# Kernel tuning notes

Hardware: AMD Instinct MI355X
Metric: run time of the kernel (lower is better)

## Reference

```python
import jax, jax.numpy as jnp
import numpy as np

ALPHA = 0.2   # leaky_relu slope inside GAT/GCN
SLOPE = 0.01  # default F.leaky_relu slope in decoder MLPs


def _leaky(x, s):
    return jnp.where(x > 0, x, s * x)


def _gat(x, mask, W, a, b):
    # AttentionLayer.forward (eval mode: attention dropout off)
    h = x @ W                                   # [N, d]
    d = W.shape[1]
    e = _leaky(h @ a[:d] + (h @ a[d:]).T, ALPHA)  # dense [N, N] scores
    att = jax.nn.softmax(jnp.where(mask > 0, e, -9e15), axis=1)
    out = _leaky(att @ h, ALPHA)
    out = out / jnp.maximum(jnp.linalg.norm(out, axis=1, keepdims=True), 1e-12)  # F.normalize p=2 dim=1
    return out + b


def reference(x, adj, gcn_W, gcn_b, hgat_W, hgat_a, hgat_b, eta,
              l1_W, l1_a, l1_b, l2_W, l2_a, l2_b, l2_rW, l2_rb,
              tf1_W, tf1_b, tf2_W, tf2_b, tg1_W, tg1_b, tg2_W, tg2_b,
              mlp_W, mlp_b, train_sample):
    N = x.shape[0]
    # normalize_adj 'sym' via row/col scaling (avoids diag matmuls)
    rowsum = adj.sum(1)
    dis = rowsum ** -0.5
    dis = jnp.where(jnp.isinf(dis), 0.0, dis)
    gcn_adj = adj * dis[:, None] * dis[None, :]
    # normalize_adj(adj,'rw') is a no-op in the source -> gat_adj = adj + I
    gat_adj = adj + jnp.eye(N, dtype=adj.dtype)

    # HybridLayer (called with gcn_adj for both branches)
    gcn_out = _leaky(gcn_adj @ (x @ gcn_W + gcn_b), 0.2)
    gat_out = _gat(x, gcn_adj, hgat_W, hgat_a, hgat_b)
    h = eta * gcn_out + (1.0 - eta) * gat_out
    h = 0.7 * h + 0.3 * jax.lax.stop_gradient(h)  # x*0.7 + x.detach()*0.3
    h = jax.nn.selu(h)

    # ConvLayer1: ResAttention heads (in==out -> identity residual), mean reduce
    h1 = jnp.mean(jnp.stack([_gat(h, gat_adj, l1_W[i], l1_a[i], l1_b[i]) + h
                             for i in range(l1_W.shape[0])]), axis=0)
    h1 = jax.nn.selu(h1)

    # ConvLayer2: ResAttention heads with linear residual projection, mean reduce
    embed = jnp.mean(jnp.stack([_gat(h1, gat_adj, l2_W[i], l2_a[i], l2_b[i])
                                + (h1 @ l2_rW[i] + l2_rb[i])
                                for i in range(l2_W.shape[0])]), axis=0)

    # decoder MLPs (eval: p=0.01 dropout omitted for determinism)
    tf = _leaky(_leaky(embed @ tf1_W + tf1_b, SLOPE) @ tf2_W + tf2_b, SLOPE)
    tg = _leaky(_leaky(embed @ tg1_W + tg1_b, SLOPE) @ tg2_W + tg2_b, SLOPE)

    pair = jnp.concatenate([tf[train_sample[:, 0]], tg[train_sample[:, 1]]], axis=1)
    return pair @ mlp_W + mlp_b  # type='MLP' decode -> [B, 2]


def setup_inputs() -> dict:
    key = jax.random.key(0)
    ks = jax.random.split(key, 32)
    N, Din, H1, H2, H3, Dout, B, NH = 6144, 512, 256, 128, 64, 32, 4096, 2
    s = 0.05
    r = lambda k, sh: (jax.random.normal(k, sh, jnp.float32) * s)
    adj = (jax.random.uniform(ks[1], (N, N)) < 0.01).astype(jnp.float32)
    return {
        'x': jax.random.normal(ks[0], (N, Din), jnp.float32),
        'adj': adj,
        'gcn_W': r(ks[2], (Din, H1)), 'gcn_b': jnp.zeros((H1,), jnp.float32),
        'hgat_W': r(ks[3], (Din, H1)), 'hgat_a': r(ks[4], (2 * H1, 1)),
        'hgat_b': jnp.zeros((H1,), jnp.float32),
        'eta': jnp.array([0.5], jnp.float32),
        'l1_W': r(ks[5], (NH, H1, H1)), 'l1_a': r(ks[6], (NH, 2 * H1, 1)),
        'l1_b': jnp.zeros((NH, H1), jnp.float32),
        'l2_W': r(ks[7], (NH, H1, H2)), 'l2_a': r(ks[8], (NH, 2 * H2, 1)),
        'l2_b': jnp.zeros((NH, H2), jnp.float32),
        'l2_rW': r(ks[9], (NH, H1, H2)), 'l2_rb': jnp.zeros((NH, H2), jnp.float32),
        'tf1_W': r(ks[10], (H2, H3)), 'tf1_b': jnp.zeros((H3,), jnp.float32),
        'tf2_W': r(ks[11], (H3, Dout)), 'tf2_b': jnp.zeros((Dout,), jnp.float32),
        'tg1_W': r(ks[12], (H2, H3)), 'tg1_b': jnp.zeros((H3,), jnp.float32),
        'tg2_W': r(ks[13], (H3, Dout)), 'tg2_b': jnp.zeros((Dout,), jnp.float32),
        'mlp_W': r(ks[14], (2 * Dout, 2)), 'mlp_b': jnp.zeros((2,), jnp.float32),
        'train_sample': jax.random.randint(ks[15], (B, 2), 0, N, jnp.int32),
    }
```

## Files before the change

kernel.cpp:

```cpp
#include <hip/hip_runtime.h>
#include <math.h>


#define NN 6144
#define CAP 256

typedef __attribute__((ext_vector_type(8))) short bf16x8;
typedef __attribute__((ext_vector_type(4))) float f32x4;

__device__ __forceinline__ unsigned short f2bf(float v) {
  unsigned u = __float_as_uint(v);
  unsigned r = u + 0x7fffu + ((u >> 16) & 1u);
  return (unsigned short)(r >> 16);
}
__device__ __forceinline__ float bf2f(unsigned short h) {
  return __uint_as_float(((unsigned)h) << 16);
}
__device__ __forceinline__ float wave_max(float v) {
#pragma unroll
  for (int off = 32; off > 0; off >>= 1) v = fmaxf(v, __shfl_xor(v, off));
  return v;
}
__device__ __forceinline__ float wave_sum(float v) {
#pragma unroll
  for (int off = 32; off > 0; off >>= 1) v += __shfl_xor(v, off);
  return v;
}
__device__ __forceinline__ float selu_f(float x) {
  const float sc = 1.0507009873554805f, al = 1.6732632423543772f;
  return x > 0.0f ? sc * x : sc * al * (__expf(x) - 1.0f);
}
__device__ __forceinline__ void write_apack4(unsigned short* __restrict__ Ah,
    unsigned short* __restrict__ Al, int KC, int m, int k0,
    float v0, float v1, float v2, float v3) {
  int mt = m >> 4, c = k0 >> 5;
  int lane = ((k0 >> 3) & 3) * 16 + (m & 15);
  int j = k0 & 7;
  size_t base = ((size_t)(mt * KC + c) * 64 + lane) * 8 + j;
  ushort4 hi, lo;
  hi.x = f2bf(v0); lo.x = f2bf(v0 - bf2f(hi.x));
  hi.y = f2bf(v1); lo.y = f2bf(v1 - bf2f(hi.y));
  hi.z = f2bf(v2); lo.z = f2bf(v2 - bf2f(hi.z));
  hi.w = f2bf(v3); lo.w = f2bf(v3 - bf2f(hi.w));
  *(ushort4*)(Ah + base) = hi;
  *(ushort4*)(Al + base) = lo;
}

__global__ __launch_bounds__(256) void build_ell(const float* __restrict__ adj,
    unsigned short* __restrict__ nbr, int* __restrict__ deg,
    int* __restrict__ selfflag, float* __restrict__ dis)
{
  __shared__ unsigned long long mS[4][6][4];
  __shared__ int cntS[4];
  __shared__ int selfS;
  int i = blockIdx.x;
  int t = threadIdx.x, lane = t & 63, w = t >> 6;
  if (t == 0) selfS = 0;
  const float* row = adj + (size_t)i * NN + w * 1536;
  int cnt = 0;
  int hasself = 0;
#pragma unroll
  for (int it = 0; it < 6; ++it) {
    float4 v = *(const float4*)(row + it * 256 + lane * 4);
    unsigned long long m0 = __ballot(v.x != 0.0f);
    unsigned long long m1 = __ballot(v.y != 0.0f);
    unsigned long long m2 = __ballot(v.z != 0.0f);
    unsigned long long m3 = __ballot(v.w != 0.0f);
    if (lane == 0) {
      mS[w][it][0] = m0; mS[w][it][1] = m1; mS[w][it][2] = m2; mS[w][it][3] = m3;
    }
    cnt += __popcll(m0) + __popcll(m1) + __popcll(m2) + __popcll(m3);
  }
  if (lane == 0) cntS[w] = cnt;
  __syncthreads();
  int base = 0;
  for (int ww = 0; ww < w; ++ww) base += cntS[ww];
  unsigned long long below = (1ull << lane) - 1ull;
#pragma unroll
  for (int it = 0; it < 6; ++it) {
    unsigned long long m0 = mS[w][it][0], m1 = mS[w][it][1];
    unsigned long long m2 = mS[w][it][2], m3 = mS[w][it][3];
    int pre = __popcll(m0 & below) + __popcll(m1 & below) +
              __popcll(m2 & below) + __popcll(m3 & below);
    int c = w * 1536 + it * 256 + lane * 4;
    int p = base + pre;
    if ((m0 >> lane) & 1) { if (p < CAP) nbr[(size_t)i * CAP + p] = (unsigned short)c;     if (c == i) hasself = 1; p++; }
    if ((m1 >> lane) & 1) { if (p < CAP) nbr[(size_t)i * CAP + p] = (unsigned short)(c+1); if (c+1 == i) hasself = 1; p++; }
    if ((m2 >> lane) & 1) { if (p < CAP) nbr[(size_t)i * CAP + p] = (unsigned short)(c+2); if (c+2 == i) hasself = 1; p++; }
    if ((m3 >> lane) & 1) { if (p < CAP) nbr[(size_t)i * CAP + p] = (unsigned short)(c+3); if (c+3 == i) hasself = 1; }
    base += __popcll(m0) + __popcll(m1) + __popcll(m2) + __popcll(m3);
  }
  if (hasself) selfS = 1;
  __syncthreads();
  if (t == 0) {
    int total = cntS[0] + cntS[1] + cntS[2] + cntS[3];
    deg[i] = total < CAP ? total : CAP;
    selfflag[i] = selfS;
    dis[i] = (total > 0) ? rsqrtf((float)total) : 0.0f;
  }
}

__global__ __launch_bounds__(256) void pack_all_b(const float* __restrict__ gcn_W,
    const float* __restrict__ hgat_W, const float* __restrict__ l1_W,
    const float* __restrict__ l2_W, const float* __restrict__ l2_rW,
    unsigned short* __restrict__ Bh, unsigned short* __restrict__ Bl)
{
  int idx = blockIdx.x * 256 + threadIdx.x;
  if (idx >= 65536) return;
  const float* B; int K, N, rel;
  if (idx < 32768) {
    B = (idx < 16384) ? gcn_W : hgat_W; K = 512; N = 256; rel = idx & 16383;
  } else if (idx < 49152) {
    B = (idx < 40960) ? l1_W : (l1_W + 65536); K = 256; N = 256; rel = (idx - 32768) & 8191;
  } else {
    int s = (idx - 49152) >> 12;
    B = (s == 0) ? l2_W : (s == 1) ? (l2_W + 32768) : (s == 2) ? l2_rW : (l2_rW + 32768);
    K = 256; N = 128; rel = (idx - 49152) & 4095;
  }
  int l = rel & 63;
  int tc = rel >> 6;
  int KC = K >> 5;
  int c = tc % KC, t = tc / KC;
  int n = t * 16 + (l & 15);
  int kb = c * 32 + (l >> 4) * 8;
  bf16x8 vh, vl;
#pragma unroll
  for (int j = 0; j < 8; ++j) {
    float v = B[(size_t)(kb + j) * N + n];
    unsigned short h = f2bf(v);
    vh[j] = (short)h;
    vl[j] = (short)f2bf(v - bf2f(h));
  }
  *(bf16x8*)(Bh + (size_t)idx * 8) = vh;
  *(bf16x8*)(Bl + (size_t)idx * 8) = vl;
}

__global__ __launch_bounds__(256) void pack_a(const float* __restrict__ A,
    unsigned short* __restrict__ Ah, unsigned short* __restrict__ Al,
    int K, int total)
{
  int idx = blockIdx.x * 256 + threadIdx.x;
  if (idx >= total) return;
  int l = idx & 63;
  int mc = idx >> 6;
  int KC = K >> 5;
  int c = mc % KC, mt = mc / KC;
  int m = mt * 16 + (l & 15);
  int kb = c * 32 + (l >> 4) * 8;
  const float* src = A + (size_t)m * K + kb;
  bf16x8 vh, vl;
#pragma unroll
  for (int j = 0; j < 8; ++j) {
    float v = src[j];
    unsigned short h = f2bf(v);
    vh[j] = (short)h;
    vl[j] = (short)f2bf(v - bf2f(h));
  }
  *(bf16x8*)(Ah + (size_t)idx * 8) = vh;
  *(bf16x8*)(Al + (size_t)idx * 8) = vl;
}

__global__ __launch_bounds__(256) void gemm_mfma(
    const unsigned short* __restrict__ Ah, const unsigned short* __restrict__ Al,
    const unsigned short* __restrict__ Bh, const unsigned short* __restrict__ Bl,
    void* C0, void* C1, void* C2, void* C3,
    const float* b0, const float* b1, const float* b2, const float* b3,
    int KC, int N, long bStride8, int obf16mask)
{
  int z = blockIdx.z;
  void* C = (z == 0) ? C0 : (z == 1) ? C1 : (z == 2) ? C2 : C3;
  const float* bias = (z == 0) ? b0 : (z == 1) ? b1 : (z == 2) ? b2 : b3;
  int obf = (obf16mask >> z) & 1;
  int wave = threadIdx.x >> 6, lane = threadIdx.x & 63;
  int mt = blockIdx.x * 4 + wave;
  int tg0 = blockIdx.y * 2;
  f32x4 acc[2];
  acc[0] = (f32x4){0.f, 0.f, 0.f, 0.f};
  acc[1] = (f32x4){0.f, 0.f, 0.f, 0.f};
  const bf16x8* ah = (const bf16x8*)Ah + (size_t)mt * KC * 64 + lane;
  const bf16x8* al = (const bf16x8*)Al + (size_t)mt * KC * 64 + lane;
  const bf16x8* bh = (const bf16x8*)Bh + (size_t)z * bStride8 + lane;
  const bf16x8* bl = (const bf16x8*)Bl + (size_t)z * bStride8 + lane;
  for (int c = 0; c < KC; ++c) {
    bf16x8 a_h = ah[c * 64];
    bf16x8 a_l = al[c * 64];
#pragma unroll
    for (int t = 0; t < 2; ++t) {
      size_t bo = (size_t)((tg0 + t) * KC + c) * 64;
      bf16x8 b_h = bh[bo];
      bf16x8 b_l = bl[bo];
      acc[t] = __builtin_amdgcn_mfma_f32_16x16x32_bf16(a_h, b_h, acc[t], 0, 0, 0);
      acc[t] = __builtin_amdgcn_mfma_f32_16x16x32_bf16(a_h, b_l, acc[t], 0, 0, 0);
      acc[t] = __builtin_amdgcn_mfma_f32_16x16x32_bf16(a_l, b_h, acc[t], 0, 0, 0);
    }
  }
  int quad = lane >> 4, cn = lane & 15;
#pragma unroll
  for (int t = 0; t < 2; ++t) {
#pragma unroll
    for (int r = 0; r < 4; ++r) {
      int row = mt * 16 + quad * 4 + r;
      int col = (tg0 + t) * 16 + cn;
      float v = acc[t][r];
      if (bias) v += bias[col];
      if (obf) ((unsigned short*)C)[(size_t)row * N + col] = f2bf(v);
      else     ((float*)C)[(size_t)row * N + col] = v;
    }
  }
}

__global__ __launch_bounds__(64) void fg_kernel(const unsigned short* __restrict__ h,
    const float* __restrict__ a, float* __restrict__ f, float* __restrict__ g,
    int d)
{
  int head = blockIdx.y;
  h += (size_t)head * NN * d;
  a += (size_t)head * 2 * d;
  f += (size_t)head * NN;
  g += (size_t)head * NN;
  int i = blockIdx.x;
  int lane = threadIdx.x;
  float sf = 0.0f, sg = 0.0f;
  for (int c = lane * 4; c < d; c += 256) {
    ushort4 hv = *(const ushort4*)(h + (size_t)i * d + c);
    float4 av = *(const float4*)(a + c);
    float4 bv = *(const float4*)(a + d + c);
    float x0 = bf2f(hv.x), x1 = bf2f(hv.y), x2 = bf2f(hv.z), x3 = bf2f(hv.w);
    sf += x0 * av.x + x1 * av.y + x2 * av.z + x3 * av.w;
    sg += x0 * bv.x + x1 * bv.y + x2 * bv.z + x3 * bv.w;
  }
  sf = wave_sum(sf);
  sg = wave_sum(sg);
  if (lane == 0) { f[i] = sf; g[i] = sg; }
}

__device__ __forceinline__ void wave_softmax(const unsigned short* __restrict__ nbr,
    int row, int dg, int klen, float fi, const float* __restrict__ g,
    const float* __restrict__ dismask,
    int lane, int& j0, int& j1, float& a0, float& a1, float* dj0, float* dj1)
{
  float e0 = -3.0e38f, e1 = -3.0e38f;
  j0 = 0; j1 = 0;
  if (lane < klen) {
    j0 = (lane < dg) ? (int)nbr[(size_t)row * CAP + lane] : row;
    float ev = fi + g[j0];
    ev = ev > 0.0f ? ev : 0.2f * ev;
    if (dismask) {
      float dj = dismask[j0];
      if (dj0) *dj0 = dj;
      if (!(dj > 0.0f)) ev = -3.0e38f;
    }
    e0 = ev;
  }
  if (lane + 64 < klen) {
    j1 = (lane + 64 < dg) ? (int)nbr[(size_t)row * CAP + lane + 64] : row;
    float ev = fi + g[j1];
    ev = ev > 0.0f ? ev : 0.2f * ev;
    if (dismask) {
      float dj = dismask[j1];
      if (dj1) *dj1 = dj;
      if (!(dj > 0.0f)) ev = -3.0e38f;
    }
    e1 = ev;
  }
  float m = wave_max(fmaxf(e0, e1));
  float x0 = (lane < klen) ? __expf(e0 - m) : 0.0f;
  float x1 = (lane + 64 < klen) ? __expf(e1 - m) : 0.0f;
  float s = wave_sum(x0 + x1);
  float inv = 1.0f / s;
  a0 = x0 * inv;
  a1 = x1 * inv;
}

template<int D, int MODE>
__global__ __launch_bounds__(256) void gat_wave(const unsigned short* __restrict__ nbr,
    const int* __restrict__ deg, const int* __restrict__ selfflag,
    const float* __restrict__ f, const float* __restrict__ g,
    const unsigned short* __restrict__ hh, const float* __restrict__ bias,
    const float* __restrict__ res,
    unsigned short* __restrict__ Ah, unsigned short* __restrict__ Al,
    float* __restrict__ emb)
{
  __shared__ float attS[4][128];
  __shared__ unsigned short jS[4][128];
  __shared__ float xchg[2][2][D];
  int t = threadIdx.x, lane = t & 63, w = t >> 6;
  int r = w & 1, head = w >> 1;
  int row = blockIdx.x * 2 + r;
  const float* fh = f + (size_t)head * NN;
  const float* gh = g + (size_t)head * NN;
  const unsigned short* hhh = hh + (size_t)head * NN * D;
  int dg = deg[row];
  int klen = dg + (selfflag[row] ? 0 : 1);
  if (klen > 128) klen = 128;
  float fi = fh[row];
  int j0, j1; float a0, a1;
  wave_softmax(nbr, row, dg, klen, fi, gh, nullptr, lane, j0, j1, a0, a1,
               nullptr, nullptr);
  if (lane < klen)      { attS[w][lane] = a0;      jS[w][lane] = (unsigned short)j0; }
  if (lane + 64 < klen) { attS[w][lane + 64] = a1; jS[w][lane + 64] = (unsigned short)j1; }

  if (MODE == 1) {
    const unsigned short* hp = hhh + 4 * lane;
    float4 acc = {0.f, 0.f, 0.f, 0.f};
    for (int k = 0; k < klen; ++k) {
      float a = attS[w][k];
      ushort4 hv = *(const ushort4*)(hp + (size_t)jS[w][k] * D);
      acc.x += a * bf2f(hv.x);
      acc.y += a * bf2f(hv.y);
      acc.z += a * bf2f(hv.z);
      acc.w += a * bf2f(hv.w);
    }
    acc.x = acc.x > 0.f ? acc.x : 0.2f * acc.x;
    acc.y = acc.y > 0.f ? acc.y : 0.2f * acc.y;
    acc.z = acc.z > 0.f ? acc.z : 0.2f * acc.z;
    acc.w = acc.w > 0.f ? acc.w : 0.2f * acc.w;
    float q = wave_sum(acc.x * acc.x + acc.y * acc.y + acc.z * acc.z + acc.w * acc.w);
    float nsc = 1.0f / fmaxf(sqrtf(q), 1e-12f);
    const float* bh = bias + (size_t)head * D + 4 * lane;
    xchg[r][head][4 * lane]     = acc.x * nsc + bh[0];
    xchg[r][head][4 * lane + 1] = acc.y * nsc + bh[1];
    xchg[r][head][4 * lane + 2] = acc.z * nsc + bh[2];
    xchg[r][head][4 * lane + 3] = acc.w * nsc + bh[3];
    __syncthreads();
    if (head == 0) {
      int c = 4 * lane;
      float4 g0 = *(const float4*)&xchg[r][0][c];
      float4 g1 = *(const float4*)&xchg[r][1][c];
      float4 hv = *(const float4*)(res + (size_t)row * D + c);
      float o0 = selu_f(0.5f * (g0.x + g1.x) + hv.x);
      float o1 = selu_f(0.5f * (g0.y + g1.y) + hv.y);
      float o2 = selu_f(0.5f * (g0.z + g1.z) + hv.z);
      float o3 = selu_f(0.5f * (g0.w + g1.w) + hv.w);
      write_apack4(Ah, Al, 8, row, c, o0, o1, o2, o3);
    }
  } else {
    const unsigned short* hp = hhh + 2 * lane;
    float ax = 0.f, ay = 0.f;
    for (int k = 0; k < klen; ++k) {
      float a = attS[w][k];
      unsigned uv = *(const unsigned*)(hp + (size_t)jS[w][k] * D);
      ax += a * bf2f((unsigned short)(uv & 0xffffu));
      ay += a * bf2f((unsigned short)(uv >> 16));
    }
    ax = ax > 0.f ? ax : 0.2f * ax;
    ay = ay > 0.f ? ay : 0.2f * ay;
    float q = wave_sum(ax * ax + ay * ay);
    float nsc = 1.0f / fmaxf(sqrtf(q), 1e-12f);
    const float* bh = bias + (size_t)head * D + 2 * lane;
    xchg[r][head][2 * lane]     = ax * nsc + bh[0];
    xchg[r][head][2 * lane + 1] = ay * nsc + bh[1];
    __syncthreads();
    if (head == 0) {
      int c = 2 * lane;
      float g0a = xchg[r][0][c],     g1a = xchg[r][1][c];
      float g0b = xchg[r][0][c + 1], g1b = xchg[r][1][c + 1];
      const float* r0 = res + (size_t)row * D + c;
      const float* r1 = res + (size_t)NN * D + (size_t)row * D + c;
      float ea = 0.5f * ((g0a + r0[0]) + (g1a + r1[0]));
      float eb = 0.5f * ((g0b + r0[1]) + (g1b + r1[1]));
      emb[(size_t)row * D + c] = ea;
      emb[(size_t)row * D + c + 1] = eb;
    }
  }
}

__global__ __launch_bounds__(256) void fused_hybrid(const unsigned short* __restrict__ nbr,
    const int* __restrict__ deg, const float* __restrict__ dis,
    const unsigned short* __restrict__ xw, const unsigned short* __restrict__ hh,
    const float* __restrict__ f, const float* __restrict__ g,
    const float* __restrict__ bias, const float* __restrict__ eta,
    float* __restrict__ hout, unsigned short* __restrict__ Ah,
    unsigned short* __restrict__ Al)
{
  __shared__ float attS[4][128];
  __shared__ float djS[4][128];
  __shared__ unsigned short jS[4][128];
  int t = threadIdx.x, lane = t & 63, w = t >> 6;
  int row = blockIdx.x * 4 + w;
  int klen = deg[row];
  if (klen > 128) klen = 128;
  float fi = f[row];
  int j0, j1; float a0, a1; float d0 = 0.f, d1 = 0.f;
  wave_softmax(nbr, row, klen, klen, fi, g, dis, lane, j0, j1, a0, a1, &d0, &d1);
  if (lane < klen)      { attS[w][lane] = a0;      djS[w][lane] = d0;      jS[w][lane] = (unsigned short)j0; }
  if (lane + 64 < klen) { attS[w][lane + 64] = a1; djS[w][lane + 64] = d1; jS[w][lane + 64] = (unsigned short)j1; }

  const unsigned short* hp = hh + 4 * lane;
  const unsigned short* xp = xw + 4 * lane;
  float4 accA = {0.f, 0.f, 0.f, 0.f};
  float4 accG = {0.f, 0.f, 0.f, 0.f};
  for (int k = 0; k < klen; ++k) {
    float a = attS[w][k];
    float dj = djS[w][k];
    size_t jo = (size_t)jS[w][k] * 256;
    ushort4 hv = *(const ushort4*)(hp + jo);
    ushort4 xv = *(const ushort4*)(xp + jo);
    accA.x += a * bf2f(hv.x); accG.x += dj * bf2f(xv.x);
    accA.y += a * bf2f(hv.y); accG.y += dj * bf2f(xv.y);
    accA.z += a * bf2f(hv.z); accG.z += dj * bf2f(xv.z);
    accA.w += a * bf2f(hv.w); accG.w += dj * bf2f(xv.w);
  }
  accA.x = accA.x > 0.f ? accA.x : 0.2f * accA.x;
  accA.y = accA.y > 0.f ? accA.y : 0.2f * accA.y;
  accA.z = accA.z > 0.f ? accA.z : 0.2f * accA.z;
  accA.w = accA.w > 0.f ? accA.w : 0.2f * accA.w;
  float q = wave_sum(accA.x * accA.x + accA.y * accA.y +
                     accA.z * accA.z + accA.w * accA.w);
  float nsc = 1.0f / fmaxf(sqrtf(q), 1e-12f);
  float di = dis[row];
  float et = eta[0];
  const float* bp = bias + 4 * lane;
  float ga[4] = {accG.x, accG.y, accG.z, accG.w};
  float at[4] = {accA.x, accA.y, accA.z, accA.w};
  float hv4[4];
#pragma unroll
  for (int u = 0; u < 4; ++u) {
    float gcn = di * ga[u];
    gcn = gcn > 0.f ? gcn : 0.2f * gcn;
    float gat = at[u] * nsc + bp[u];
    float z = et * gcn + (1.0f - et) * gat;
    hv4[u] = selu_f(z);
  }
  *(float4*)(hout + (size_t)row * 256 + 4 * lane) =
      (float4){hv4[0], hv4[1], hv4[2], hv4[3]};
  write_apack4(Ah, Al, 8, row, 4 * lane, hv4[0], hv4[1], hv4[2], hv4[3]);
}

__global__ __launch_bounds__(256) void decoder_fused(const float* __restrict__ emb,
    const float* __restrict__ tf1_W, const float* __restrict__ tf1_b,
    const float* __restrict__ tf2_W, const float* __restrict__ tf2_b,
    const float* __restrict__ tg1_W, const float* __restrict__ tg1_b,
    const float* __restrict__ tg2_W, const float* __restrict__ tg2_b,
    float* __restrict__ TF, float* __restrict__ TG)
{
  __shared__ float embS[128 * 16];
  __shared__ float t1S[128 * 16];
  int t = threadIdx.x;
  int r0 = blockIdx.x * 16;
  for (int e = t; e < 2048; e += 256) {
    int r = e >> 7, k = e & 127;
    embS[k * 16 + r] = emb[(size_t)(r0 + r) * 128 + k];
  }
  __syncthreads();
  int c = t & 127, half = t >> 7;
  const float* W1 = (c < 64) ? tf1_W : tg1_W;
  int c1 = c & 63;
  float b1v = (c < 64) ? tf1_b[c1] : tg1_b[c1];
  float acc1[8];
#pragma unroll
  for (int r = 0; r < 8; ++r) acc1[r] = b1v;
  for (int k = 0; k < 128; ++k) {
    float wv = W1[k * 64 + c1];
#pragma unroll
    for (int r = 0; r < 8; ++r) acc1[r] += wv * embS[k * 16 + half * 8 + r];
  }
#pragma unroll
  for (int r = 0; r < 8; ++r) {
    float v = acc1[r];
    t1S[c * 16 + half * 8 + r] = v > 0.0f ? v : 0.01f * v;
  }
  __syncthreads();
  int c2 = t & 63, rg = t >> 6;
  const float* W2 = (c2 < 32) ? tf2_W : tg2_W;
  int cc = c2 & 31;
  float b2v = (c2 < 32) ? tf2_b[cc] : tg2_b[cc];
  int koff = (c2 < 32) ? 0 : 64;
  float acc2[4];
#pragma unroll
  for (int r = 0; r < 4; ++r) acc2[r] = b2v;
  for (int k = 0; k < 64; ++k) {
    float wv = W2[k * 32 + cc];
#pragma unroll
    for (int r = 0; r < 4; ++r) acc2[r] += wv * t1S[(koff + k) * 16 + rg * 4 + r];
  }
  float* O = (c2 < 32) ? TF : TG;
#pragma unroll
  for (int r = 0; r < 4; ++r) {
    float v = acc2[r];
    v = v > 0.0f ? v : 0.01f * v;
    O[(size_t)(r0 + rg * 4 + r) * 32 + cc] = v;
  }
}

__global__ void decode_mlp(const float* __restrict__ tf,
    const float* __restrict__ tg, const int* __restrict__ samp,
    const float* __restrict__ W, const float* __restrict__ b,
    float* __restrict__ out, int B)
{
  int bid = blockIdx.x * blockDim.x + threadIdx.x;
  if (bid >= B) return;
  int s0 = samp[2 * bid], s1 = samp[2 * bid + 1];
  float a0 = b[0], a1 = b[1];
#pragma unroll
  for (int c = 0; c < 32; ++c) {
    float v = tf[(size_t)s0 * 32 + c];
    a0 += v * W[2 * c];
    a1 += v * W[2 * c + 1];
  }
#pragma unroll
  for (int c = 0; c < 32; ++c) {
    float v = tg[(size_t)s1 * 32 + c];
    a0 += v * W[2 * (32 + c)];
    a1 += v * W[2 * (32 + c) + 1];
  }
  out[2 * bid] = a0;
  out[2 * bid + 1] = a1;
}

extern "C" void kernel_launch(void* const* d_in, const int* in_sizes, int n_in,
                              void* d_out, int out_size, void* d_ws, size_t ws_size,
                              hipStream_t stream)
{
  const float* x      = (const float*)d_in[0];
  const float* adj    = (const float*)d_in[1];
  const float* gcn_W  = (const float*)d_in[2];
  const float* gcn_b  = (const float*)d_in[3];
  const float* hgat_W = (const float*)d_in[4];
  const float* hgat_a = (const float*)d_in[5];
  const float* hgat_b = (const float*)d_in[6];
  const float* eta    = (const float*)d_in[7];
  const float* l1_W   = (const float*)d_in[8];
  const float* l1_a   = (const float*)d_in[9];
  const float* l1_b   = (const float*)d_in[10];
  const float* l2_W   = (const float*)d_in[11];
  const float* l2_a   = (const float*)d_in[12];
  const float* l2_b   = (const float*)d_in[13];
  const float* l2_rW  = (const float*)d_in[14];
  const float* l2_rb  = (const float*)d_in[15];
  const float* tf1_W  = (const float*)d_in[16];
  const float* tf1_b  = (const float*)d_in[17];
  const float* tf2_W  = (const float*)d_in[18];
  const float* tf2_b  = (const float*)d_in[19];
  const float* tg1_W  = (const float*)d_in[20];
  const float* tg1_b  = (const float*)d_in[21];
  const float* tg2_W  = (const float*)d_in[22];
  const float* tg2_b  = (const float*)d_in[23];
  const float* mlp_W  = (const float*)d_in[24];
  const float* mlp_b  = (const float*)d_in[25];
  const int*   samp   = (const int*)d_in[26];
  float* out = (float*)d_out;

  char* ws = (char*)d_ws;
  size_t off = 0;
  auto alloc = [&](size_t bytes) -> void* {
    void* p = ws + off;
    off += (bytes + 255) & ~(size_t)255;
    return p;
  };
  unsigned short* nbr = (unsigned short*)alloc((size_t)NN * CAP * 2);
  int*   deg = (int*)  alloc((size_t)NN * 4);
  int*   sfl = (int*)  alloc((size_t)NN * 4);
  float* dis = (float*)alloc((size_t)NN * 4);
  float* fv  = (float*)alloc((size_t)2 * NN * 4);
  float* gv  = (float*)alloc((size_t)2 * NN * 4);
  unsigned short* H0b = (unsigned short*)alloc((size_t)2 * NN * 256 * 2);
  float* Hh  = (float*)alloc((size_t)NN * 256 * 4);
  unsigned short* HHb = (unsigned short*)alloc((size_t)2 * NN * 256 * 2);
  unsigned short* Qb  = (unsigned short*)alloc((size_t)2 * NN * 128 * 2);
  float* Qr  = (float*)alloc((size_t)2 * NN * 128 * 4);
  float* emb = (float*)alloc((size_t)NN * 128 * 4);
  float* TF  = (float*)alloc((size_t)NN * 32 * 4);
  float* TG  = (float*)alloc((size_t)NN * 32 * 4);
  unsigned short* APH = (unsigned short*)alloc((size_t)NN * 512 * 2);
  unsigned short* APL = (unsigned short*)alloc((size_t)NN * 512 * 2);
  unsigned short* BPH = (unsigned short*)alloc((size_t)65536 * 8 * 2);
  unsigned short* BPL = (unsigned short*)alloc((size_t)65536 * 8 * 2);
  (void)ws_size; (void)n_in; (void)in_sizes; (void)out_size;

  const float* nil = nullptr;

  build_ell<<<NN, 256, 0, stream>>>(adj, nbr, deg, sfl, dis);
  pack_all_b<<<256, 256, 0, stream>>>(gcn_W, hgat_W, l1_W, l2_W, l2_rW, BPH, BPL);
  const int tA512 = (NN / 16) * 16 * 64;
  pack_a<<<tA512 / 256, 256, 0, stream>>>(x, APH, APL, 512, tA512);

  gemm_mfma<<<dim3(96, 8, 2), 256, 0, stream>>>(APH, APL, BPH, BPL,
      H0b, H0b + (size_t)NN * 256, nullptr, nullptr, gcn_b, nil, nil, nil,
      16, 256, 16384, 0x3);
  fg_kernel<<<dim3(NN, 1), 64, 0, stream>>>(H0b + (size_t)NN * 256, hgat_a, fv, gv, 256);
  fused_hybrid<<<NN / 4, 256, 0, stream>>>(nbr, deg, dis, H0b, H0b + (size_t)NN * 256,
      fv, gv, hgat_b, eta, Hh, APH, APL);

  gemm_mfma<<<dim3(96, 8, 2), 256, 0, stream>>>(APH, APL, BPH + (size_t)32768 * 8,
      BPL + (size_t)32768 * 8, HHb, HHb + (size_t)NN * 256, nullptr, nullptr,
      nil, nil, nil, nil, 8, 256, 8192, 0x3);
  fg_kernel<<<dim3(NN, 2), 64, 0, stream>>>(HHb, l1_a, fv, gv, 256);
  gat_wave<256, 1><<<NN / 2, 256, 0, stream>>>(nbr, deg, sfl, fv, gv, HHb, l1_b,
      Hh, APH, APL, nullptr);

  gemm_mfma<<<dim3(96, 4, 4), 256, 0, stream>>>(APH, APL, BPH + (size_t)49152 * 8,
      BPL + (size_t)49152 * 8,
      Qb, Qb + (size_t)NN * 128, Qr, Qr + (size_t)NN * 128,
      nil, nil, l2_rb, l2_rb + 128, 8, 128, 4096, 0x3);
  fg_kernel<<<dim3(NN, 2), 64, 0, stream>>>(Qb, l2_a, fv, gv, 128);
  gat_wave<128, 2><<<NN / 2, 256, 0, stream>>>(nbr, deg, sfl, fv, gv, Qb, l2_b,
      Qr, nullptr, nullptr, emb);

  decoder_fused<<<NN / 16, 256, 0, stream>>>(emb, tf1_W, tf1_b, tf2_W, tf2_b,
      tg1_W, tg1_b, tg2_W, tg2_b, TF, TG);

  decode_mlp<<<16, 256, 0, stream>>>(TF, TG, samp, mlp_W, mlp_b, out, 4096);
}
```

Measured before the change: 436.5 us.

## Fuse attention score projections into GEMM epilogue and merge pack kernels

Removes the three separate fg_kernel launches by computing the f/g attention dot products inside the GEMM epilogue. Each wave reduces its partial products across 16 lanes with shuffles and accumulates them into zero-initialized buffers with atomicAdd. The separate A-packing and weight-packing kernels are merged into one launch that also zeroes those f/g buffers. In exchange, f/g use fp32 pre-rounding values, and atomic accumulation order makes the sums nondeterministic. It also adds atomic traffic across the column-tile blocks.

```diff
diff --git a/kernel.cpp b/kernel.cpp
--- a/kernel.cpp
+++ b/kernel.cpp
@@ -100,13 +100,37 @@
   }
 }
 
-__global__ __launch_bounds__(256) void pack_all_b(const float* __restrict__ gcn_W,
+__global__ __launch_bounds__(256) void pack_all(const float* __restrict__ gcn_W,
     const float* __restrict__ hgat_W, const float* __restrict__ l1_W,
     const float* __restrict__ l2_W, const float* __restrict__ l2_rW,
-    unsigned short* __restrict__ Bh, unsigned short* __restrict__ Bl)
+    const float* __restrict__ x,
+    unsigned short* __restrict__ Bh, unsigned short* __restrict__ Bl,
+    unsigned short* __restrict__ Ah, unsigned short* __restrict__ Al,
+    float* __restrict__ fgZ)
 {
   int idx = blockIdx.x * 256 + threadIdx.x;
-  if (idx >= 65536) return;
+  if (idx >= 520192) return;
+  if (idx >= 458752) { fgZ[idx - 458752] = 0.0f; return; }
+  if (idx >= 65536) {
+    int rel = idx - 65536;
+    int l = rel & 63;
+    int mc = rel >> 6;
+    int c = mc & 15, mt = mc >> 4;
+    int m = mt * 16 + (l & 15);
+    int kb = c * 32 + (l >> 4) * 8;
+    const float* src = x + (size_t)m * 512 + kb;
+    bf16x8 vh, vl;
+#pragma unroll
+    for (int j = 0; j < 8; ++j) {
+      float v = src[j];
+      unsigned short h = f2bf(v);
+      vh[j] = (short)h;
+      vl[j] = (short)f2bf(v - bf2f(h));
+    }
+    *(bf16x8*)(Ah + (size_t)rel * 8) = vh;
+    *(bf16x8*)(Al + (size_t)rel * 8) = vl;
+    return;
+  }
   const float* B; int K, N, rel;
   if (idx < 32768) {
     B = (idx < 16384) ? gcn_W : hgat_W; K = 512; N = 256; rel = idx & 16383;
@@ -135,37 +159,14 @@
   *(bf16x8*)(Bl + (size_t)idx * 8) = vl;
 }
 
-__global__ __launch_bounds__(256) void pack_a(const float* __restrict__ A,
-    unsigned short* __restrict__ Ah, unsigned short* __restrict__ Al,
-    int K, int total)
-{
-  int idx = blockIdx.x * 256 + threadIdx.x;
-  if (idx >= total) return;
-  int l = idx & 63;
-  int mc = idx >> 6;
-  int KC = K >> 5;
-  int c = mc % KC, mt = mc / KC;
-  int m = mt * 16 + (l & 15);
-  int kb = c * 32 + (l >> 4) * 8;
-  const float* src = A + (size_t)m * K + kb;
-  bf16x8 vh, vl;
-#pragma unroll
-  for (int j = 0; j < 8; ++j) {
-    float v = src[j];
-    unsigned short h = f2bf(v);
-    vh[j] = (short)h;
-    vl[j] = (short)f2bf(v - bf2f(h));
-  }
-  *(bf16x8*)(Ah + (size_t)idx * 8) = vh;
-  *(bf16x8*)(Al + (size_t)idx * 8) = vl;
-}
-
 __global__ __launch_bounds__(256) void gemm_mfma(
     const unsigned short* __restrict__ Ah, const unsigned short* __restrict__ Al,
     const unsigned short* __restrict__ Bh, const unsigned short* __restrict__ Bl,
     void* C0, void* C1, void* C2, void* C3,
     const float* b0, const float* b1, const float* b2, const float* b3,
-    int KC, int N, long bStride8, int obf16mask)
+    int KC, int N, long bStride8, int obf16mask,
+    int fgmask, const float* __restrict__ aBase,
+    float* __restrict__ fBase, float* __restrict__ gBase)
 {
   int z = blockIdx.z;
   void* C = (z == 0) ? C0 : (z == 1) ? C1 : (z == 2) ? C2 : C3;
@@ -197,41 +198,38 @@
   int quad = lane >> 4, cn = lane & 15;
 #pragma unroll
   for (int t = 0; t < 2; ++t) {
+    int col = (tg0 + t) * 16 + cn;
+    float bv = bias ? bias[col] : 0.0f;
 #pragma unroll
     for (int r = 0; r < 4; ++r) {
       int row = mt * 16 + quad * 4 + r;
-      int col = (tg0 + t) * 16 + cn;
-      float v = acc[t][r];
-      if (bias) v += bias[col];
+      float v = acc[t][r] + bv;
+      acc[t][r] = v;
       if (obf) ((unsigned short*)C)[(size_t)row * N + col] = f2bf(v);
       else     ((float*)C)[(size_t)row * N + col] = v;
     }
   }
-}
-
-__global__ __launch_bounds__(64) void fg_kernel(const unsigned short* __restrict__ h,
-    const float* __restrict__ a, float* __restrict__ f, float* __restrict__ g,
-    int d)
-{
-  int head = blockIdx.y;
-  h += (size_t)head * NN * d;
-  a += (size_t)head * 2 * d;
-  f += (size_t)head * NN;
-  g += (size_t)head * NN;
-  int i = blockIdx.x;
-  int lane = threadIdx.x;
-  float sf = 0.0f, sg = 0.0f;
-  for (int c = lane * 4; c < d; c += 256) {
-    ushort4 hv = *(const ushort4*)(h + (size_t)i * d + c);
-    float4 av = *(const float4*)(a + c);
-    float4 bv = *(const float4*)(a + d + c);
-    float x0 = bf2f(hv.x), x1 = bf2f(hv.y), x2 = bf2f(hv.z), x3 = bf2f(hv.w);
-    sf += x0 * av.x + x1 * av.y + x2 * av.z + x3 * av.w;
-    sg += x0 * bv.x + x1 * bv.y + x2 * bv.z + x3 * bv.w;
-  }
-  sf = wave_sum(sf);
-  sg = wave_sum(sg);
-  if (lane == 0) { f[i] = sf; g[i] = sg; }
+  if ((fgmask >> z) & 1) {
+    const float* af = aBase + (size_t)z * 2 * N;
+    const float* ag = af + N;
+    float af0 = af[tg0 * 16 + cn], af1 = af[(tg0 + 1) * 16 + cn];
+    float ag0 = ag[tg0 * 16 + cn], ag1 = ag[(tg0 + 1) * 16 + cn];
+#pragma unroll
+    for (int r = 0; r < 4; ++r) {
+      float pf = acc[0][r] * af0 + acc[1][r] * af1;
+      float pg = acc[0][r] * ag0 + acc[1][r] * ag1;
+#pragma unroll
+      for (int off = 1; off < 16; off <<= 1) {
+        pf += __shfl_xor(pf, off);
+        pg += __shfl_xor(pg, off);
+      }
+      if (cn == 0) {
+        int row = mt * 16 + quad * 4 + r;
+        atomicAdd(fBase + (size_t)z * NN + row, pf);
+        atomicAdd(gBase + (size_t)z * NN + row, pg);
+      }
+    }
+  }
 }
 
 __device__ __forceinline__ void wave_softmax(const unsigned short* __restrict__ nbr,
@@ -552,8 +550,7 @@
   int*   deg = (int*)  alloc((size_t)NN * 4);
   int*   sfl = (int*)  alloc((size_t)NN * 4);
   float* dis = (float*)alloc((size_t)NN * 4);
-  float* fv  = (float*)alloc((size_t)2 * NN * 4);
-  float* gv  = (float*)alloc((size_t)2 * NN * 4);
+  float* fgZ = (float*)alloc((size_t)10 * NN * 4);
   unsigned short* H0b = (unsigned short*)alloc((size_t)2 * NN * 256 * 2);
   float* Hh  = (float*)alloc((size_t)NN * 256 * 4);
   unsigned short* HHb = (unsigned short*)alloc((size_t)2 * NN * 256 * 2);
@@ -568,33 +565,39 @@
   unsigned short* BPL = (unsigned short*)alloc((size_t)65536 * 8 * 2);
   (void)ws_size; (void)n_in; (void)in_sizes; (void)out_size;
 
+  float* fv0 = fgZ;
+  float* gv0 = fgZ + NN;
+  float* fv1 = fgZ + 2 * NN;
+  float* gv1 = fgZ + 4 * NN;
+  float* fv2 = fgZ + 6 * NN;
+  float* gv2 = fgZ + 8 * NN;
+
   const float* nil = nullptr;
 
   build_ell<<<NN, 256, 0, stream>>>(adj, nbr, deg, sfl, dis);
-  pack_all_b<<<256, 256, 0, stream>>>(gcn_W, hgat_W, l1_W, l2_W, l2_rW, BPH, BPL);
-  const int tA512 = (NN / 16) * 16 * 64;
-  pack_a<<<tA512 / 256, 256, 0, stream>>>(x, APH, APL, 512, tA512);
+  pack_all<<<2032, 256, 0, stream>>>(gcn_W, hgat_W, l1_W, l2_W, l2_rW, x,
+      BPH, BPL, APH, APL, fgZ);
 
   gemm_mfma<<<dim3(96, 8, 2), 256, 0, stream>>>(APH, APL, BPH, BPL,
       H0b, H0b + (size_t)NN * 256, nullptr, nullptr, gcn_b, nil, nil, nil,
-      16, 256, 16384, 0x3);
-  fg_kernel<<<dim3(NN, 1), 64, 0, stream>>>(H0b + (size_t)NN * 256, hgat_a, fv, gv, 256);
+      16, 256, 16384, 0x3,
+      0x2, hgat_a - 512, fv0 - NN, gv0 - NN);
   fused_hybrid<<<NN / 4, 256, 0, stream>>>(nbr, deg, dis, H0b, H0b + (size_t)NN * 256,
-      fv, gv, hgat_b, eta, Hh, APH, APL);
+      fv0, gv0, hgat_b, eta, Hh, APH, APL);
 
   gemm_mfma<<<dim3(96, 8, 2), 256, 0, stream>>>(APH, APL, BPH + (size_t)32768 * 8,
       BPL + (size_t)32768 * 8, HHb, HHb + (size_t)NN * 256, nullptr, nullptr,
-      nil, nil, nil, nil, 8, 256, 8192, 0x3);
-  fg_kernel<<<dim3(NN, 2), 64, 0, stream>>>(HHb, l1_a, fv, gv, 256);
-  gat_wave<256, 1><<<NN / 2, 256, 0, stream>>>(nbr, deg, sfl, fv, gv, HHb, l1_b,
+      nil, nil, nil, nil, 8, 256, 8192, 0x3,
+      0x3, l1_a, fv1, gv1);
+  gat_wave<256, 1><<<NN / 2, 256, 0, stream>>>(nbr, deg, sfl, fv1, gv1, HHb, l1_b,
       Hh, APH, APL, nullptr);
 
   gemm_mfma<<<dim3(96, 4, 4), 256, 0, stream>>>(APH, APL, BPH + (size_t)49152 * 8,
       BPL + (size_t)49152 * 8,
       Qb, Qb + (size_t)NN * 128, Qr, Qr + (size_t)NN * 128,
-      nil, nil, l2_rb, l2_rb + 128, 8, 128, 4096, 0x3);
-  fg_kernel<<<dim3(NN, 2), 64, 0, stream>>>(Qb, l2_a, fv, gv, 128);
-  gat_wave<128, 2><<<NN / 2, 256, 0, stream>>>(nbr, deg, sfl, fv, gv, Qb, l2_b,
+      nil, nil, l2_rb, l2_rb + 128, 8, 128, 4096, 0x3,
+      0x3, l2_a, fv2, gv2);
+  gat_wave<128, 2><<<NN / 2, 256, 0, stream>>>(nbr, deg, sfl, fv2, gv2, Qb, l2_b,
       Qr, nullptr, nullptr, emb);
 
   decoder_fused<<<NN / 16, 256, 0, stream>>>(emb, tf1_W, tf1_b, tf2_W, tf2_b,
```

After: 427.3 us. 2.1% less time.
